# Performance work log

Measured on AMD Instinct MI355X. Metric: run time of the kernel, lower is better.

## Reference

```python
import jax, jax.numpy as jnp
import numpy as np

B, L, D_MODEL = 8, 1024, 512
D_STATE, D_CONV, EXPAND = 16, 4, 2
D_INNER = EXPAND * D_MODEL          # 1024
DT_RANK = (D_MODEL + 15) // 16      # 32
D_FF = 4 * D_MODEL                  # 2048
EPS = 1e-12


def setup_inputs() -> dict:
    key = jax.random.key(0)
    ks = jax.random.split(key, 16)
    s = 0.02
    n = lambda k, shp: jax.random.normal(k, shp, dtype=jnp.float32) * s
    A = jnp.tile(jnp.arange(1, D_STATE + 1, dtype=jnp.float32)[None, :], (D_INNER, 1))
    return {
        "x": jax.random.normal(ks[0], (B, L, D_MODEL), dtype=jnp.float32),
        "in_proj_w": n(ks[1], (2 * D_INNER, D_MODEL)),
        "conv_w": n(ks[2], (D_INNER, 1, D_CONV)),
        "conv_b": jnp.zeros((D_INNER,), jnp.float32),
        "x_proj_w": n(ks[3], (DT_RANK + 2 * D_STATE, D_INNER)),
        "dt_proj_w": n(ks[4], (D_INNER, DT_RANK)),
        "dt_proj_b": jnp.full((D_INNER,), -4.0, jnp.float32),  # softplus(~-4) -> small dt
        "A_log": jnp.log(A),
        "D": jnp.ones((D_INNER,), jnp.float32),
        "out_proj_w": n(ks[5], (D_MODEL, D_INNER)),
        "ln1_g": jnp.ones((D_MODEL,), jnp.float32),
        "ln1_b": jnp.zeros((D_MODEL,), jnp.float32),
        "fc1_w": n(ks[6], (D_FF, D_MODEL)),
        "fc1_b": jnp.zeros((D_FF,), jnp.float32),
        "fc2_w": n(ks[7], (D_MODEL, D_FF)),
        "fc2_b": jnp.zeros((D_MODEL,), jnp.float32),
        "ln2_g": jnp.ones((D_MODEL,), jnp.float32),
        "ln2_b": jnp.zeros((D_MODEL,), jnp.float32),
    }


def _layernorm(x, g, b):
    m = jnp.mean(x, axis=-1, keepdims=True)
    v = jnp.var(x, axis=-1, keepdims=True)
    return (x - m) * jax.lax.rsqrt(v + EPS) * g + b


def _mamba(x, in_proj_w, conv_w, conv_b, x_proj_w, dt_proj_w, dt_proj_b, A_log, D, out_proj_w):
    # in_proj: [B,L,d_model] -> [B,L,2*d_inner]
    xz = jnp.einsum("bld,ed->ble", x, in_proj_w)
    u, z = jnp.split(xz, 2, axis=-1)                      # each [B,L,d_inner]
    # depthwise causal conv over time
    uc = jax.lax.conv_general_dilated(
        jnp.transpose(u, (0, 2, 1)), conv_w,
        window_strides=(1,), padding=[(D_CONV - 1, 0)],
        feature_group_count=D_INNER,
        dimension_numbers=("NCH", "OIH", "NCH"))
    u = jnp.transpose(uc, (0, 2, 1)) + conv_b             # [B,L,d_inner]
    u = jax.nn.silu(u)
    # x_proj -> dt, B, C
    x_dbl = jnp.einsum("bld,ed->ble", u, x_proj_w)
    dt, Bm, Cm = jnp.split(x_dbl, [DT_RANK, DT_RANK + D_STATE], axis=-1)
    dt = jax.nn.softplus(jnp.einsum("blr,dr->bld", dt, dt_proj_w) + dt_proj_b)  # [B,L,d_inner]
    A = -jnp.exp(A_log)                                   # [d_inner, d_state]
    deltaA = jnp.exp(dt[..., None] * A)                   # [B,L,d_inner,d_state]
    deltaBu = dt[..., None] * Bm[:, :, None, :] * u[..., None]

    def step(h, inp):
        dA_t, dBu_t, C_t = inp                            # [B,di,ds],[B,di,ds],[B,ds]
        h = h * dA_t + dBu_t
        y = jnp.einsum("bds,bs->bd", h, C_t)
        return h, y

    h0 = jnp.zeros((x.shape[0], D_INNER, D_STATE), x.dtype)
    _, ys = jax.lax.scan(step, h0, (jnp.transpose(deltaA, (1, 0, 2, 3)),
                                    jnp.transpose(deltaBu, (1, 0, 2, 3)),
                                    jnp.transpose(Cm, (1, 0, 2))))
    y = jnp.transpose(ys, (1, 0, 2)) + u * D              # [B,L,d_inner]
    y = y * jax.nn.silu(z)
    return jnp.einsum("ble,de->bld", y, out_proj_w)


def reference(x, in_proj_w, conv_w, conv_b, x_proj_w, dt_proj_w, dt_proj_b, A_log, D,
              out_proj_w, ln1_g, ln1_b, fc1_w, fc1_b, fc2_w, fc2_b, ln2_g, ln2_b):
    h = _mamba(x, in_proj_w, conv_w, conv_b, x_proj_w, dt_proj_w, dt_proj_b,
               A_log, D, out_proj_w)
    h = _layernorm(h + x, ln1_g, ln1_b)                   # dropout = identity (eval)
    # FeedForward with residual + LayerNorm
    f = jax.nn.gelu(jnp.einsum("bld,fd->blf", h, fc1_w) + fc1_b, approximate=False)
    f = jnp.einsum("blf,df->bld", f, fc2_w) + fc2_b
    return _layernorm(f + h, ln2_g, ln2_b)
```

## Files before the change

kernel.cpp:

```cpp
#include <hip/hip_runtime.h>
#include <hip/hip_bf16.h>
#include <math.h>

typedef __hip_bfloat16 bf16;
typedef unsigned short u16;
typedef unsigned int u32;
typedef __attribute__((ext_vector_type(8))) short short8;
typedef __attribute__((ext_vector_type(4))) float f32x4;
typedef __attribute__((ext_vector_type(4))) u32 u32x4;

#define B_  8
#define L_  1024
#define DM  512
#define DI  1024
#define DS  16
#define DR  32
#define DF  2048
#define M_  (B_ * L_)

__device__ __forceinline__ float b2f(bf16 x) { return __bfloat162float(x); }
__device__ __forceinline__ bf16  f2b(float x) { return __float2bfloat16(x); }
__device__ __forceinline__ u16   bu(bf16 x)  { return __builtin_bit_cast(u16, x); }
__device__ __forceinline__ float s2f(short x) { return b2f(__builtin_bit_cast(bf16, (u16)x)); }
__device__ __forceinline__ float uphi(u32 w) { return __builtin_bit_cast(float, w & 0xffff0000u); }
__device__ __forceinline__ float uplo(u32 w) { return __builtin_bit_cast(float, w << 16); }

__device__ __forceinline__ bool is_b16(const void* flag) {
    return ((const u16*)flag)[0] == 0x3F80;
}
__device__ __forceinline__ float ldr(const void* p, size_t i, bool b16) {
    return b16 ? b2f(((const bf16*)p)[i]) : ((const float*)p)[i];
}

__device__ __forceinline__ float fexp2(float x) {
#if __has_builtin(__builtin_amdgcn_exp2f)
    return __builtin_amdgcn_exp2f(x);
#else
    return __expf(x * 0.6931471805599453f);
#endif
}

__device__ __forceinline__ float fsoftplus(float v) {
    return (v > 20.f) ? v : __logf(1.f + __expf(v));
}

__device__ __forceinline__ float fgelu(float v) {
    const float x = v * 0.7071067811865475f;
    const float ax = fabsf(x);
    const float t = __builtin_amdgcn_rcpf(fmaf(0.3275911f, ax, 1.f));
    float p = fmaf(1.061405429f, t, -1.453152027f);
    p = fmaf(p, t, 1.421413741f);
    p = fmaf(p, t, -0.284496736f);
    p = fmaf(p, t, 0.254829592f);
    const float e = __expf(-ax * ax);
    float erf = 1.f - p * t * e;
    erf = (x < 0.f) ? -erf : erf;
    return 0.5f * v * (1.f + erf);
}

__device__ __forceinline__ void gload16(const bf16* g, bf16* l) {
    __builtin_amdgcn_global_load_lds(
        (const __attribute__((address_space(1))) unsigned int*)g,
        (__attribute__((address_space(3))) unsigned int*)l, 16, 0, 0);
}

__device__ __forceinline__ float fsilu(float x) {
    return x * __builtin_amdgcn_rcpf(1.f + __expf(-x));
}

#define CN0 (M_ * DM)
#define CN1 (CN0 + 2 * DI * DM)
#define CN2 (CN1 + 64 * DI)
#define CN3 (CN2 + DI * DR)
#define CN4 (CN3 + DM * DI)
#define CN5 (CN4 + DF * DM)
#define CN6 (CN5 + DM * DF)
#define CN7 (CN6 + DI * 4)
#define CN8 (CN7 + DI)
#define CN9 (CN8 + DI)
__global__ __launch_bounds__(256) void cvt_all_kernel(
    const void* s0, const void* s1, const void* s2, const void* s3,
    const void* s4, const void* s5, const void* s6, const void* s7,
    const void* s8, const void* s9,
    bf16* __restrict__ dst)
{
    const long i = ((long)blockIdx.x * 256 + threadIdx.x) * 8;
    if (i >= CN9) return;
    const void* src; long off;
    if      (i < CN0) { src = s0; off = i; }
    else if (i < CN1) { src = s1; off = i - CN0; }
    else if (i < CN2) { src = s2; off = i - CN1; }
    else if (i < CN3) { src = s3; off = i - CN2; }
    else if (i < CN4) { src = s4; off = i - CN3; }
    else if (i < CN5) { src = s5; off = i - CN4; }
    else if (i < CN6) { src = s6; off = i - CN5; }
    else if (i < CN7) { src = s7; off = i - CN6; }
    else if (i < CN8) { src = s8; off = i - CN7; }
    else              { src = s9; off = i - CN8; }
    const float* f = (const float*)src + off;
    const f32x4 a = *(const f32x4*)f;
    const f32x4 b = *(const f32x4*)(f + 4);
    short8 o;
#pragma unroll
    for (int k = 0; k < 4; ++k) {
        o[k]     = (short)bu(f2b(a[k]));
        o[k + 4] = (short)bu(f2b(b[k]));
    }
    *(short8*)(dst + i) = o;
}

template <int BM, int BN, int NT, int ACT, int PACK>
__global__ __launch_bounds__(NT) void mfma_gemm(
    const bf16* __restrict__ A, int lda,
    const bf16* __restrict__ W, int ldw,
    const void* __restrict__ bias,
    bf16* __restrict__ C, int ldc,
    int K, const void* __restrict__ flag,
    void* __restrict__ pk, void* __restrict__ pk2,
    const bf16* __restrict__ uin)
{
    constexpr int WN = (BN >= 128) ? 2 : 1;
    constexpr int CA = BM * 4 / NT;
    constexpr int CB = BN * 4 / NT;
    constexpr int BUF = (BM + BN) * 32;
    __shared__ __align__(16) bf16 smem[2 * BUF];
    const int tid  = threadIdx.x;
    const int wave = tid >> 6, lane = tid & 63;
    const int quad = lane >> 4, l16 = lane & 15;
    const u32 gx  = gridDim.x;
    const u32 nwg = gx * gridDim.y;
    const u32 lid = blockIdx.y * gx + blockIdx.x;
    const u32 swz = (lid & 7) * (nwg >> 3) + (lid >> 3);
    const int bm = (int)(swz / gx) * BM, bn = (int)(swz % gx) * BN;
    const int wm = (wave / WN) * 64, wn = (wave % WN) * 64;

    f32x4 acc[4][4];
#pragma unroll
    for (int i = 0; i < 4; ++i)
#pragma unroll
        for (int j = 0; j < 4; ++j) acc[i][j] = (f32x4){0.f, 0.f, 0.f, 0.f};

    auto load_tile = [&](int k0, int p) {
        bf16* As = smem + p * BUF;
        bf16* Ws = As + BM * 32;
#pragma unroll
        for (int j = 0; j < CA; ++j) {
            const int e = j * NT + tid;
            gload16(A + (size_t)(bm + (e >> 2)) * lda + k0 + (e & 3) * 8, As + e * 8);
        }
#pragma unroll
        for (int j = 0; j < CB; ++j) {
            const int e = j * NT + tid;
            gload16(W + (size_t)(bn + (e >> 2)) * ldw + k0 + (e & 3) * 8, Ws + e * 8);
        }
    };

    const int NIT = K >> 5;
    load_tile(0, 0);
    for (int it = 0; it < NIT; ++it) {
        __syncthreads();
        if (it + 1 < NIT) load_tile((it + 1) << 5, (it + 1) & 1);
        const bf16* As = smem + (it & 1) * BUF;
        const bf16* Ws = As + BM * 32;
        short8 af[4], wf[4];
#pragma unroll
        for (int mt = 0; mt < 4; ++mt)
            af[mt] = *(const short8*)(As + (wm + mt * 16 + l16) * 32 + quad * 8);
#pragma unroll
        for (int nt = 0; nt < 4; ++nt)
            wf[nt] = *(const short8*)(Ws + (wn + nt * 16 + l16) * 32 + quad * 8);
#pragma unroll
        for (int mt = 0; mt < 4; ++mt)
#pragma unroll
            for (int nt = 0; nt < 4; ++nt)
                acc[mt][nt] = __builtin_amdgcn_mfma_f32_16x16x32_bf16(
                    af[mt], wf[nt], acc[mt][nt], 0, 0, 0);
    }

    const bool b16 = bias ? is_b16(flag) : false;
#pragma unroll
    for (int nt = 0; nt < 4; ++nt) {
        const int col = bn + wn + nt * 16 + l16;
        const float bv = bias ? ldr(bias, col, b16) : 0.f;
#pragma unroll
        for (int mt = 0; mt < 4; ++mt)
#pragma unroll
            for (int i = 0; i < 4; ++i) {
                const int row = bm + wm + mt * 16 + quad * 4 + i;
                float v = acc[mt][nt][i] + bv;
                if (ACT == 1) v = fsoftplus(v);
                else if (ACT == 2) v = fgelu(v);
                C[(size_t)row * ldc + col] = f2b(v);
            }
    }
    if (PACK == 2) {
#pragma unroll
        for (int mt = 0; mt < 4; ++mt)
#pragma unroll
            for (int i = 0; i < 4; ++i) {
                const int row = bm + wm + mt * 16 + quad * 4 + i;
                ((float*)pk)[(size_t)row * 16 + l16]  = acc[mt][2][i];
                ((float*)pk2)[(size_t)row * 16 + l16] = acc[mt][3][i];
            }
    }
}

__global__ __launch_bounds__(256) void conv_silu_kernel(
    const bf16* __restrict__ xz,
    const bf16* __restrict__ cw,
    const bf16* __restrict__ cb,
    const bf16* __restrict__ Dw,
    bf16* __restrict__ u,
    u32* __restrict__ ug)
{
    const int t  = blockIdx.x * 256 + threadIdx.x;
    const long t8 = (long)t * 8;
    const int d8  = (int)(t8 & (DI - 1));
    const int row = (int)(t8 >> 10);
    const int l   = row & (L_ - 1);

    short8 wraw[4];
#pragma unroll
    for (int k = 0; k < 4; ++k)
        wraw[k] = *(const short8*)(cw + (size_t)d8 * 4 + k * 8);
    const short8 cbv = *(const short8*)(cb + d8);
    const short8 dv  = *(const short8*)(Dw + d8);

    float acc[8];
#pragma unroll
    for (int i = 0; i < 8; ++i) acc[i] = s2f(cbv[i]);
#pragma unroll
    for (int j = 0; j < 4; ++j) {
        const int ls = l - 3 + j;
        if (ls >= 0) {
            const short8 xv = *(const short8*)(xz + (size_t)(row - 3 + j) * (2 * DI) + d8);
#pragma unroll
            for (int i = 0; i < 8; ++i) {
                const int f = i * 4 + j;
                acc[i] += s2f(wraw[f >> 3][f & 7]) * s2f(xv[i]);
            }
        }
    }
    const short8 zv = *(const short8*)(xz + (size_t)row * (2 * DI) + DI + d8);
    short8 us;
    u32x4 g0, g1;
#pragma unroll
    for (int i = 0; i < 8; ++i) {
        const float uv = fsilu(acc[i]);
        us[i] = (short)bu(f2b(uv));
        const float gz = fsilu(s2f(zv[i]));
        const float g2 = uv * s2f(dv[i]) * gz;
        const u32 p = ((u32)bu(f2b(g2)) << 16) | bu(f2b(gz));
        if (i < 4) g0[i] = p; else g1[i - 4] = p;
    }
    *(short8*)(u + t8) = us;
    *(u32x4*)(ug + t8) = g0;
    *(u32x4*)(ug + t8 + 4) = g1;
}

__global__ __launch_bounds__(256) void scan_kernel(
    const bf16* __restrict__ xdbl,
    const bf16* __restrict__ u,
    const float* __restrict__ Bf,
    const float* __restrict__ Cf,
    const u32* __restrict__ ug,
    const void* __restrict__ A_log,
    const bf16* __restrict__ dtw,
    const void* __restrict__ dt_b,
    bf16* __restrict__ y,
    const void* __restrict__ flag)
{
    const bool b16 = is_b16(flag);
    const int tid = threadIdx.x;
    const int lane = tid & 63;
    const int s  = lane & 15;
    const int dl = tid >> 4;
    const int quad = dl & 3;
    const int v = tid >> 6;
    const int b = blockIdx.x >> 6, dch = blockIdx.x & 63;
    const int d0 = dch * 16, d = d0 + dl;
    const float AcL = -__expf(ldr(A_log, (size_t)d * DS + s, b16))
                      * 1.4426950408889634f;

    const short8 wfrag = *(const short8*)(dtw + (size_t)(d0 + s) * DR + quad * 8);
    const float dtb = ldr(dt_b, d0 + s, b16);

    __shared__ __align__(16) float dt_s[16][68];
    __shared__ __align__(16) float du_s[16][68];
    __shared__ __align__(16) float B_s[16][68];
    __shared__ __align__(16) float C_s[16][68];
    __shared__ u32 ug_s[16][68];
    __shared__ bf16 y_s[16][72];
    __shared__ float p_s[16][16][33];

    const int c16 = tid & 15, r16 = tid >> 4;
    float rB[4], rC[4];
    u32 rug[4];
    short8 rxd;
    u16 ru4[4];
    const size_t base = (size_t)b * L_;

    auto load_chunk = [&](int l0) {
#pragma unroll
        for (int j = 0; j < 4; ++j) {
            const size_t row = base + l0 + r16 + 16 * j;
            rug[j] = ug[row * DI + d0 + c16];
            rB[j]  = Bf[row * 16 + c16];
            rC[j]  = Cf[row * 16 + c16];
        }
        rxd = *(const short8*)(xdbl + (size_t)(base + l0 + v * 16 + s) * 64
                               + quad * 8);
#pragma unroll
        for (int i = 0; i < 4; ++i)
            ru4[i] = ((const u16*)u)[(size_t)(base + l0 + v * 16 + quad * 4 + i)
                                     * DI + d0 + s];
    };
    auto store_chunk = [&]() {
#pragma unroll
        for (int j = 0; j < 4; ++j) {
            ug_s[c16][r16 + 16 * j] = rug[j];
            B_s[c16][r16 + 16 * j]  = rB[j];
            C_s[c16][r16 + 16 * j]  = rC[j];
        }
        f32x4 a0 = __builtin_amdgcn_mfma_f32_16x16x32_bf16(
            rxd, wfrag, (f32x4){0.f, 0.f, 0.f, 0.f}, 0, 0, 0);
        f32x4 dtv, duv;
#pragma unroll
        for (int i = 0; i < 4; ++i) {
            const float t = fsoftplus(a0[i] + dtb);
            dtv[i] = t;
            duv[i] = t * s2f((short)ru4[i]);
        }
        *(f32x4*)&dt_s[s][v * 16 + quad * 4] = dtv;
        *(f32x4*)&du_s[s][v * 16 + quad * 4] = duv;
    };

    float h = 0.f;
    float* const prow = &p_s[dl][s][0];
    load_chunk(0);
    for (int c = 0; c < 16; ++c) {
        store_chunk();
        __syncthreads();
        if (c < 15) load_chunk((c + 1) * 64);
#pragma unroll
        for (int g = 0; g < 2; ++g) {
#pragma unroll
            for (int w2 = 0; w2 < 2; ++w2) {
                const int w = g * 2 + w2;
                f32x4 dtw4[4], duw[4], bw[4], cw[4];
#pragma unroll
                for (int q = 0; q < 4; ++q) {
                    dtw4[q] = *(const f32x4*)&dt_s[dl][w * 16 + q * 4];
                    duw[q]  = *(const f32x4*)&du_s[dl][w * 16 + q * 4];
                    bw[q]   = *(const f32x4*)&B_s[s][w * 16 + q * 4];
                    cw[q]   = *(const f32x4*)&C_s[s][w * 16 + q * 4];
                }
#pragma unroll
                for (int t = 0; t < 16; ++t) {
                    const float e = fexp2(dtw4[t >> 2][t & 3] * AcL);
                    h = fmaf(h, e, duw[t >> 2][t & 3] * bw[t >> 2][t & 3]);
                    prow[w2 * 16 + t] = h * cw[t >> 2][t & 3];
                }
            }
            asm volatile("s_waitcnt lgkmcnt(0)" ::: "memory");
#pragma unroll
            for (int w2 = 0; w2 < 2; ++w2) {
                const int w = g * 2 + w2;
                const u32 ugw = ug_s[dl][w * 16 + s];
                float pr[16];
#pragma unroll
                for (int k = 0; k < 16; ++k) pr[k] = p_s[dl][k][w2 * 16 + s];
#pragma unroll
                for (int o = 8; o >= 1; o >>= 1)
#pragma unroll
                    for (int i = 0; i < o; ++i) pr[i] += pr[i + o];
                y_s[dl][w * 16 + s] = f2b(fmaf(pr[0], uplo(ugw), uphi(ugw)));
            }
        }
        __syncthreads();
#pragma unroll
        for (int j = 0; j < 4; ++j) {
            const size_t row = base + c * 64 + r16 + 16 * j;
            y[row * DI + d0 + c16] = y_s[c16][r16 + 16 * j];
        }
    }
}

template <int RMODE, int OMODE>
__global__ __launch_bounds__(256) void ln_kernel(
    const bf16* __restrict__ inp,
    const bf16* __restrict__ res,
    const void* __restrict__ g,
    const void* __restrict__ bb,
    void* __restrict__ out,
    const void* __restrict__ flag)
{
    const bool b16 = is_b16(flag);
    const int wv = threadIdx.x >> 6, lane = threadIdx.x & 63;
    const int row = blockIdx.x * 4 + wv;
    const size_t off = (size_t)row * DM;
    const int e = lane * 8;

    float v[8];
    const short8 iv = *(const short8*)(inp + off + e);
    const short8 rv = *(const short8*)(res + off + e);
#pragma unroll
    for (int i = 0; i < 8; ++i) v[i] = s2f(iv[i]) + s2f(rv[i]);

    float sum = 0.f, sq = 0.f;
#pragma unroll
    for (int i = 0; i < 8; ++i) { sum += v[i]; sq += v[i] * v[i]; }
#pragma unroll
    for (int o = 32; o >= 1; o >>= 1) {
        sum += __shfl_xor(sum, o);
        sq  += __shfl_xor(sq, o);
    }
    const float m = sum * (1.f / DM);
    const float var = sq * (1.f / DM) - m * m;
    const float inv = rsqrtf(fmaxf(var, 0.f) + 1e-12f);

    float gv[8], bv[8];
    if (b16) {
        const short8 gg = *(const short8*)((const bf16*)g + e);
        const short8 bg = *(const short8*)((const bf16*)bb + e);
#pragma unroll
        for (int i = 0; i < 8; ++i) { gv[i] = s2f(gg[i]); bv[i] = s2f(bg[i]); }
    } else {
        const float* gf = (const float*)g + e;
        const float* bf = (const float*)bb + e;
        const f32x4 g0 = *(const f32x4*)gf, g1 = *(const f32x4*)(gf + 4);
        const f32x4 b0 = *(const f32x4*)bf, b1 = *(const f32x4*)(bf + 4);
#pragma unroll
        for (int i = 0; i < 8; ++i) {
            gv[i] = i < 4 ? g0[i] : g1[i - 4];
            bv[i] = i < 4 ? b0[i] : b1[i - 4];
        }
    }
    float o[8];
#pragma unroll
    for (int i = 0; i < 8; ++i) o[i] = (v[i] - m) * inv * gv[i] + bv[i];

    if (OMODE == 2 && !b16) {
        f32x4 o0, o1;
#pragma unroll
        for (int i = 0; i < 4; ++i) { o0[i] = o[i]; o1[i] = o[i + 4]; }
        *(f32x4*)((float*)out + off + e) = o0;
        *(f32x4*)((float*)out + off + e + 4) = o1;
    } else {
        short8 os;
#pragma unroll
        for (int i = 0; i < 8; ++i) os[i] = (short)bu(f2b(o[i]));
        *(short8*)((bf16*)out + off + e) = os;
    }
}

extern "C" void kernel_launch(void* const* d_in, const int* in_sizes, int n_in,
                              void* d_out, int out_size, void* d_ws, size_t ws_size,
                              hipStream_t stream)
{
    (void)n_in; (void)out_size; (void)ws_size;
    const void* x       = d_in[0];
    const void* in_w    = d_in[1];
    const void* conv_w  = d_in[2];
    const void* conv_b  = d_in[3];
    const void* xproj_w = d_in[4];
    const void* dt_w    = d_in[5];
    const void* dt_b    = d_in[6];
    const void* A_log   = d_in[7];
    const void* Dw      = d_in[8];
    const void* out_w   = d_in[9];
    const void* ln1_g   = d_in[10];
    const void* ln1_b   = d_in[11];
    const void* fc1_w   = d_in[12];
    const void* fc1_b   = d_in[13];
    const void* fc2_w   = d_in[14];
    const void* fc2_b   = d_in[15];
    const void* ln2_g   = d_in[16];
    const void* ln2_b   = d_in[17];
    const void* flag    = ln1_g;

    const bool hb16 = (in_sizes[0] == (int)(M_ * DM * sizeof(bf16)));

    bf16* xb    = (bf16*)d_ws;
    bf16* inwb  = xb    + (size_t)M_ * DM;
    bf16* xpwb  = inwb  + (size_t)2 * DI * DM;
    bf16* dtwb  = xpwb  + (size_t)64 * DI;
    bf16* outwb = dtwb  + (size_t)DI * DR;
    bf16* fc1wb = outwb + (size_t)DM * DI;
    bf16* fc2wb = fc1wb + (size_t)DF * DM;
    bf16* cwb   = fc2wb + (size_t)DM * DF;
    bf16* cbb   = cwb   + (size_t)DI * 4;
    bf16* dwb   = cbb   + (size_t)DI;
    bf16* xz    = dwb   + (size_t)DI;
    bf16* u     = xz    + (size_t)M_ * 2 * DI;
    bf16* xdbl  = u     + (size_t)M_ * DI;
    float* dtf  = (float*)(xdbl + (size_t)M_ * 64);
    u32*  ugp   = (u32*)(dtf + (size_t)M_ * DI);
    float* Bfp  = (float*)(ugp + (size_t)M_ * DI);
    bf16* yb    = (bf16*)(Bfp + (size_t)M_ * 16);
    bf16* hb    = yb    + (size_t)M_ * DI;
    float* Cfp  = (float*)hb;
    bf16* mo    = (bf16*)dtf;
    bf16* fb    = xz;
    bf16* f2b_  = yb;

    const bf16 *xp, *inwp, *xpwp, *dtwp, *outwp, *fc1p, *fc2p, *cwp, *cbp, *dwp;
    dim3 blk(256);
    if (hb16) {
        xp   = (const bf16*)x;       inwp = (const bf16*)in_w;
        xpwp = (const bf16*)xproj_w; dtwp = (const bf16*)dt_w;
        outwp = (const bf16*)out_w;  fc1p = (const bf16*)fc1_w;
        fc2p = (const bf16*)fc2_w;   cwp  = (const bf16*)conv_w;
        cbp  = (const bf16*)conv_b;  dwp  = (const bf16*)Dw;
    } else {
        cvt_all_kernel<<<dim3((CN9 / 8 + 255) / 256), blk, 0, stream>>>(
            x, in_w, xproj_w, dt_w, out_w, fc1_w, fc2_w, conv_w, conv_b, Dw,
            xb);
        xp = xb; inwp = inwb; xpwp = xpwb; dtwp = dtwb; outwp = outwb;
        fc1p = fc1wb; fc2p = fc2wb; cwp = cwb; cbp = cbb; dwp = dwb;
    }

    mfma_gemm<128, 128, 256, 0, 0><<<dim3(16, 64), blk, 0, stream>>>(
        xp, DM, inwp, DM, nullptr, xz, 2 * DI, DM, flag, nullptr, nullptr, nullptr);
    conv_silu_kernel<<<dim3(M_ * DI / 8 / 256), blk, 0, stream>>>(
        xz, cwp, cbp, dwp, u, ugp);
    mfma_gemm<128, 64, 128, 0, 2><<<dim3(1, 64), dim3(128), 0, stream>>>(
        u, DI, xpwp, DI, nullptr, xdbl, 64, DI, flag, Bfp, Cfp, nullptr);
    scan_kernel<<<dim3(B_ * 64), blk, 0, stream>>>(
        xdbl, u, Bfp, Cfp, ugp, A_log, dtwp, dt_b, yb, flag);
    mfma_gemm<128, 128, 256, 0, 0><<<dim3(4, 64), blk, 0, stream>>>(
        yb, DI, outwp, DI, nullptr, mo, DM, DI, flag, nullptr, nullptr, nullptr);
    ln_kernel<1, 1><<<dim3(M_ / 4), blk, 0, stream>>>(
        mo, xp, ln1_g, ln1_b, hb, flag);
    mfma_gemm<128, 128, 256, 2, 0><<<dim3(16, 64), blk, 0, stream>>>(
        hb, DM, fc1p, DM, fc1_b, fb, DF, DM, flag, nullptr, nullptr, nullptr);
    mfma_gemm<128, 128, 256, 0, 0><<<dim3(4, 64), blk, 0, stream>>>(
        fb, DF, fc2p, DF, fc2_b, f2b_, DM, DF, flag, nullptr, nullptr, nullptr);
    ln_kernel<1, 2><<<dim3(M_ / 4), blk, 0, stream>>>(
        f2b_, hb, ln2_g, ln2_b, d_out, flag);
}
```

Before: 325.3 us.

## Compute z-gate and D-skip inside scan instead of materializing ug buffer

The conv kernel no longer computes silu(z) or the u*D*silu(z) term, and no longer writes the packed 32-bit ug buffer. The scan kernel instead reads z from xz and u directly, then computes the gate values while staging them into shared memory. This cuts one full-size intermediate write and read, at the cost of extra strided 16-bit loads and some extra math in the scan. Separately, the x_proj GEMM changes from 128x64 tiles on 128 threads to 64x64 tiles on 64 threads with twice the blocks.

```diff
diff --git a/kernel.cpp b/kernel.cpp
--- a/kernel.cpp
+++ b/kernel.cpp
@@ -209,9 +209,7 @@
     const bf16* __restrict__ xz,
     const bf16* __restrict__ cw,
     const bf16* __restrict__ cb,
-    const bf16* __restrict__ Dw,
-    bf16* __restrict__ u,
-    u32* __restrict__ ug)
+    bf16* __restrict__ u)
 {
     const int t  = blockIdx.x * 256 + threadIdx.x;
     const long t8 = (long)t * 8;
@@ -224,7 +222,6 @@
     for (int k = 0; k < 4; ++k)
         wraw[k] = *(const short8*)(cw + (size_t)d8 * 4 + k * 8);
     const short8 cbv = *(const short8*)(cb + d8);
-    const short8 dv  = *(const short8*)(Dw + d8);
 
     float acc[8];
 #pragma unroll
@@ -241,32 +238,23 @@
             }
         }
     }
-    const short8 zv = *(const short8*)(xz + (size_t)row * (2 * DI) + DI + d8);
     short8 us;
-    u32x4 g0, g1;
-#pragma unroll
-    for (int i = 0; i < 8; ++i) {
-        const float uv = fsilu(acc[i]);
-        us[i] = (short)bu(f2b(uv));
-        const float gz = fsilu(s2f(zv[i]));
-        const float g2 = uv * s2f(dv[i]) * gz;
-        const u32 p = ((u32)bu(f2b(g2)) << 16) | bu(f2b(gz));
-        if (i < 4) g0[i] = p; else g1[i - 4] = p;
-    }
+#pragma unroll
+    for (int i = 0; i < 8; ++i)
+        us[i] = (short)bu(f2b(fsilu(acc[i])));
     *(short8*)(u + t8) = us;
-    *(u32x4*)(ug + t8) = g0;
-    *(u32x4*)(ug + t8 + 4) = g1;
 }
 
 __global__ __launch_bounds__(256) void scan_kernel(
     const bf16* __restrict__ xdbl,
     const bf16* __restrict__ u,
+    const bf16* __restrict__ xz,
     const float* __restrict__ Bf,
     const float* __restrict__ Cf,
-    const u32* __restrict__ ug,
     const void* __restrict__ A_log,
     const bf16* __restrict__ dtw,
     const void* __restrict__ dt_b,
+    const bf16* __restrict__ Dw,
     bf16* __restrict__ y,
     const void* __restrict__ flag)
 {
@@ -284,6 +272,7 @@
 
     const short8 wfrag = *(const short8*)(dtw + (size_t)(d0 + s) * DR + quad * 8);
     const float dtb = ldr(dt_b, d0 + s, b16);
+    const float Dd  = b2f(Dw[d0 + s]);
 
     __shared__ __align__(16) float dt_s[16][68];
     __shared__ __align__(16) float du_s[16][68];
@@ -295,7 +284,7 @@
 
     const int c16 = tid & 15, r16 = tid >> 4;
     float rB[4], rC[4];
-    u32 rug[4];
+    u16 rz[4], ru2[4];
     short8 rxd;
     u16 ru4[4];
     const size_t base = (size_t)b * L_;
@@ -304,7 +293,8 @@
 #pragma unroll
         for (int j = 0; j < 4; ++j) {
             const size_t row = base + l0 + r16 + 16 * j;
-            rug[j] = ug[row * DI + d0 + c16];
+            rz[j]  = ((const u16*)xz)[row * (2 * DI) + DI + d0 + c16];
+            ru2[j] = ((const u16*)u)[row * DI + d0 + c16];
             rB[j]  = Bf[row * 16 + c16];
             rC[j]  = Cf[row * 16 + c16];
         }
@@ -318,7 +308,10 @@
     auto store_chunk = [&]() {
 #pragma unroll
         for (int j = 0; j < 4; ++j) {
-            ug_s[c16][r16 + 16 * j] = rug[j];
+            const float uv = s2f((short)ru2[j]);
+            const float gz = fsilu(s2f((short)rz[j]));
+            const float g2 = uv * Dd * gz;
+            ug_s[c16][r16 + 16 * j] = ((u32)bu(f2b(g2)) << 16) | bu(f2b(gz));
             B_s[c16][r16 + 16 * j]  = rB[j];
             C_s[c16][r16 + 16 * j]  = rC[j];
         }
@@ -523,11 +516,11 @@
     mfma_gemm<128, 128, 256, 0, 0><<<dim3(16, 64), blk, 0, stream>>>(
         xp, DM, inwp, DM, nullptr, xz, 2 * DI, DM, flag, nullptr, nullptr, nullptr);
     conv_silu_kernel<<<dim3(M_ * DI / 8 / 256), blk, 0, stream>>>(
-        xz, cwp, cbp, dwp, u, ugp);
-    mfma_gemm<128, 64, 128, 0, 2><<<dim3(1, 64), dim3(128), 0, stream>>>(
+        xz, cwp, cbp, u);
+    mfma_gemm<64, 64, 64, 0, 2><<<dim3(1, 128), dim3(64), 0, stream>>>(
         u, DI, xpwp, DI, nullptr, xdbl, 64, DI, flag, Bfp, Cfp, nullptr);
     scan_kernel<<<dim3(B_ * 64), blk, 0, stream>>>(
-        xdbl, u, Bfp, Cfp, ugp, A_log, dtwp, dt_b, yb, flag);
+        xdbl, u, xz, Bfp, Cfp, A_log, dtwp, dt_b, dwp, yb, flag);
     mfma_gemm<128, 128, 256, 0, 0><<<dim3(4, 64), blk, 0, stream>>>(
         yb, DI, outwp, DI, nullptr, mo, DM, DI, flag, nullptr, nullptr, nullptr);
     ln_kernel<1, 1><<<dim3(M_ / 4), blk, 0, stream>>>(
```

After: 320.5 us, median of 2. Within noise of the previous version (-1.5%).
